# Optimization experiments

Measured on AMD Instinct MI355X. Metric: run time of the kernel, lower is better.

Reference implementation:

```python
import jax, jax.numpy as jnp
import numpy as np

B, S, D, H = 4, 1500, 1280, 20
HD = D // H  # 64

def setup_inputs() -> dict:
    key = jax.random.key(0)
    ks = jax.random.split(key, 8)
    scale = 1.0 / np.sqrt(D)
    return {
        "hidden_states": jax.random.normal(ks[0], (B, S, D), dtype=jnp.float32),
        "attention_mask": jnp.zeros((B, 1, S, S), dtype=jnp.float32),
        "q_w": jax.random.normal(ks[1], (D, D), dtype=jnp.float32) * scale,
        "q_b": jax.random.normal(ks[2], (D,), dtype=jnp.float32) * 0.02,
        "k_w": jax.random.normal(ks[3], (D, D), dtype=jnp.float32) * scale,
        "v_w": jax.random.normal(ks[4], (D, D), dtype=jnp.float32) * scale,
        "v_b": jax.random.normal(ks[5], (D,), dtype=jnp.float32) * 0.02,
        "o_w": jax.random.normal(ks[6], (D, D), dtype=jnp.float32) * scale,
        "o_b": jax.random.normal(ks[7], (D,), dtype=jnp.float32) * 0.02,
    }

def reference(hidden_states, attention_mask, q_w, q_b, k_w, v_w, v_b, o_w, o_b):
    bsz, seq_len, d_model = hidden_states.shape
    scaling = HD ** (-0.5)
    # Projections (k_proj has NO bias, matching the module)
    q = hidden_states @ q_w + q_b
    k = hidden_states @ k_w
    v = hidden_states @ v_w + v_b
    # [B, H, S, HD]
    q = q.reshape(bsz, seq_len, H, HD).transpose(0, 2, 1, 3)
    k = k.reshape(bsz, seq_len, H, HD).transpose(0, 2, 1, 3)
    v = v.reshape(bsz, seq_len, H, HD).transpose(0, 2, 1, 3)
    scores = jnp.einsum("bhqd,bhkd->bhqk", q, k) * scaling
    scores = scores + attention_mask
    attn = jax.nn.softmax(scores.astype(jnp.float32), axis=-1).astype(q.dtype)
    out = jnp.einsum("bhqk,bhkd->bhqd", attn, v)
    out = out.transpose(0, 2, 1, 3).reshape(bsz, seq_len, d_model)
    return out @ o_w + o_b
```

## Files before the change

### kernel.cpp

```cpp
#include <hip/hip_runtime.h>
#include <hip/hip_bf16.h>
#include <cstddef>

#define B_   4
#define S_   1500
#define D_   1280
#define H_   20
#define HD_  64
#define M_   (B_*S_)
#define SPAD 1536
#define BIGNEG (-1e30f)
#define LOG2E 1.44269504088896340736f
#define KVB  64
#define NTA  24

typedef short bf16x8 __attribute__((ext_vector_type(8)));
typedef float f32x4 __attribute__((ext_vector_type(4)));
typedef unsigned short u16;
typedef u16 u16x8 __attribute__((ext_vector_type(8)));
typedef unsigned int u32x4v __attribute__((ext_vector_type(4)));

#define MFMA __builtin_amdgcn_mfma_f32_16x16x32_bf16

__device__ __forceinline__ u16 f2bf(float f) {
  union { float f; unsigned u; } x; x.f = f;
  unsigned r = (x.u + 0x7fffu + ((x.u >> 16) & 1u)) >> 16;
  return (u16)r;
}

__device__ __forceinline__ unsigned cvtpk(float a, float b) {
  unsigned r;
  asm volatile("v_cvt_pk_bf16_f32 %0, %1, %2" : "=v"(r) : "v"(a), "v"(b));
  return r;
}

__device__ __forceinline__ void gl_lds16(const u16* g, u16* l) {
  typedef __attribute__((address_space(1))) const unsigned GU;
  typedef __attribute__((address_space(3))) unsigned LU;
  __builtin_amdgcn_global_load_lds((GU*)g, (LU*)l, 16, 0, 0);
}

__global__ __launch_bounds__(256) void k_conv(const float* __restrict__ X, u16* __restrict__ Y) {
  size_t i = (size_t)blockIdx.x * 256 + threadIdx.x;
  const float4* p = (const float4*)(X + i * 8);
  float4 a = p[0], b = p[1];
  u16x8 v;
  v[0]=f2bf(a.x); v[1]=f2bf(a.y); v[2]=f2bf(a.z); v[3]=f2bf(a.w);
  v[4]=f2bf(b.x); v[5]=f2bf(b.y); v[6]=f2bf(b.z); v[7]=f2bf(b.w);
  *(u16x8*)(Y + i * 8) = v;
}

__global__ __launch_bounds__(256) void k_trans4(const float* __restrict__ qw,
                                                const float* __restrict__ kw,
                                                const float* __restrict__ vw,
                                                const float* __restrict__ ow,
                                                u16* __restrict__ Wt) {
  const float* W = (blockIdx.z == 0) ? qw : (blockIdx.z == 1) ? kw
                   : (blockIdx.z == 2) ? vw : ow;
  u16* dst = Wt + (size_t)blockIdx.z * D_ * D_;
  __shared__ float t[32][33];
  int n0 = blockIdx.x * 32, k0 = blockIdx.y * 32;
  int tx = threadIdx.x & 31, ty = threadIdx.x >> 5;
  #pragma unroll
  for (int i = ty; i < 32; i += 8) t[i][tx] = W[(size_t)(k0 + i) * D_ + n0 + tx];
  __syncthreads();
  #pragma unroll
  for (int i = ty; i < 32; i += 8) dst[(size_t)(n0 + i) * D_ + k0 + tx] = f2bf(t[tx][i]);
}

__global__ __launch_bounds__(256) void k_vtrans(const u16* __restrict__ Vb, u16* __restrict__ Vt) {
  __shared__ u16 t[128][72];
  int bh = blockIdx.x, b = bh / H_, h = bh % H_;
  int s0 = blockIdx.y * 128;
  int tid = threadIdx.x;
  #pragma unroll
  for (int r = 0; r < 4; r++) {
    int sl = r * 32 + (tid >> 3);
    int s = s0 + sl; if (s > S_ - 1) s = S_ - 1;
    bf16x8 v = *(const bf16x8*)(Vb + ((size_t)(b * S_ + s)) * D_ + h * HD_ + (tid & 7) * 8);
    *(bf16x8*)&t[sl][(tid & 7) * 8] = v;
  }
  __syncthreads();
  #pragma unroll
  for (int r = 0; r < 4; r++) {
    int d = r * 16 + (tid >> 4);
    int ss = (tid & 15) * 8;
    u16x8 o;
    #pragma unroll
    for (int q = 0; q < 8; q++) {
      int sl = ss + q;
      int kk = ((sl >> 4) & 3) * 4 + (sl & 3) + ((sl >> 2) & 3) * 16 + (sl & 64);
      o[q] = t[kk][d];
    }
    *(u16x8*)(Vt + ((size_t)bh * HD_ + d) * SPAD + s0 + ss) = o;
  }
}

__global__ __launch_bounds__(256) void k_gemmqkv(const u16* __restrict__ A,
                                                 const u16* __restrict__ Wt,
                                                 const float* __restrict__ q_b,
                                                 const float* __restrict__ v_b,
                                                 u16* __restrict__ Qb) {
  __shared__ u16 As[2][128 * 64];
  __shared__ u16 Bs[2][128 * 64];
  int tid = threadIdx.x;
  int lane = tid & 63;
  int wv = tid >> 6;
  int l16 = lane & 15, lg = lane >> 4;
  int wr = wv >> 1, wc = wv & 1;
  int m0 = blockIdx.x * 128;
  int n0g = blockIdx.y * 128;
  int sel = blockIdx.y / 10;
  int nloc = n0g - sel * 1280;

  int srow = tid >> 3;
  int csw = ((tid & 7) ^ (srow & 7)) * 8;
  const u16* asrc = A + csw;
  const u16* bsrc = Wt + csw;
  int dbase = wv * 8 * 64;

  f32x4 acc[4][4] = {};

#define STAGEG(tt, bufb) do {                                            \
    int kk0 = (tt) * 64;                                                 \
    _Pragma("unroll")                                                    \
    for (int c = 0; c < 4; c++) {                                        \
      int row = srow + c * 32;                                           \
      int ar = m0 + row; if (ar > M_ - 1) ar = M_ - 1;                   \
      gl_lds16(asrc + (size_t)ar * D_ + kk0,                             \
               &As[bufb][0] + dbase + c * 2048);                         \
      gl_lds16(bsrc + (size_t)(n0g + row) * D_ + kk0,                    \
               &Bs[bufb][0] + dbase + c * 2048);                         \
    }                                                                    \
  } while (0)

  STAGEG(0, 0);
  __syncthreads();
  for (int t = 0; t < 20; t++) {
    int cb = t & 1;
    if (t < 19) STAGEG(t + 1, cb ^ 1);
    const u16* AsC = &As[cb][0];
    const u16* BsC = &Bs[cb][0];
    #pragma unroll
    for (int kk = 0; kk < 2; kk++) {
      int pcol = ((kk * 4 + lg) ^ (l16 & 7)) * 8;
      bf16x8 af[4], bf[4];
      #pragma unroll
      for (int m = 0; m < 4; m++)
        af[m] = *(const bf16x8*)&AsC[(wr * 64 + m * 16 + l16) * 64 + pcol];
      #pragma unroll
      for (int n = 0; n < 4; n++)
        bf[n] = *(const bf16x8*)&BsC[(wc * 64 + n * 16 + l16) * 64 + pcol];
      __builtin_amdgcn_s_setprio(1);
      #pragma unroll
      for (int m = 0; m < 4; m++)
        #pragma unroll
        for (int n = 0; n < 4; n++)
          acc[m][n] = MFMA(af[m], bf[n], acc[m][n], 0, 0, 0);
      __builtin_amdgcn_s_setprio(0);
    }
    __syncthreads();
  }
#undef STAGEG

  const float* bias = (sel == 0) ? q_b : v_b;
  float scl = (sel == 0) ? (0.125f * LOG2E) : 1.0f;
  u16* outb = Qb + (size_t)sel * ((size_t)M_ * D_);

  #pragma unroll
  for (int m = 0; m < 4; m++) {
    int row0 = m0 + wr * 64 + m * 16 + lg * 4;
    #pragma unroll
    for (int n = 0; n < 4; n++) {
      int colL = nloc + wc * 64 + n * 16 + l16;
      float bv = (sel == 1) ? 0.0f : bias[colL];
      #pragma unroll
      for (int j = 0; j < 4; j++) {
        int row = row0 + j;
        if (row < M_) {
          float v = (acc[m][n][j] + bv) * scl;
          outb[(size_t)row * D_ + colL] = f2bf(v);
        }
      }
    }
  }
}

__global__ __launch_bounds__(256) void k_gemmo(const u16* __restrict__ A,
                                               const u16* __restrict__ Wt,
                                               const float* __restrict__ bias,
                                               float* __restrict__ outp) {
  __shared__ u16 As[2][128 * 64];
  __shared__ u16 Bs[2][128 * 64];
  int tid = threadIdx.x;
  int lane = tid & 63;
  int wv = tid >> 6;
  int l16 = lane & 15, lg = lane >> 4;
  int wr = wv >> 1, wc = wv & 1;
  int m0 = blockIdx.x * 128, n0 = blockIdx.y * 128;

  int srow = tid >> 3;
  int csw = ((tid & 7) ^ (srow & 7)) * 8;
  const u16* asrc = A + csw;
  const u16* bsrc = Wt + csw;
  int dbase = wv * 8 * 64;

  f32x4 acc[4][4] = {};

#define STAGEG(tt, bufb) do {                                            \
    int kk0 = (tt) * 64;                                                 \
    _Pragma("unroll")                                                    \
    for (int c = 0; c < 4; c++) {                                        \
      int row = srow + c * 32;                                           \
      int ar = m0 + row; if (ar > M_ - 1) ar = M_ - 1;                   \
      gl_lds16(asrc + (size_t)ar * D_ + kk0,                             \
               &As[bufb][0] + dbase + c * 2048);                         \
      gl_lds16(bsrc + (size_t)(n0 + row) * D_ + kk0,                     \
               &Bs[bufb][0] + dbase + c * 2048);                         \
    }                                                                    \
  } while (0)

  STAGEG(0, 0);
  __syncthreads();
  for (int t = 0; t < 20; t++) {
    int cb = t & 1;
    if (t < 19) STAGEG(t + 1, cb ^ 1);
    const u16* AsC = &As[cb][0];
    const u16* BsC = &Bs[cb][0];
    #pragma unroll
    for (int kk = 0; kk < 2; kk++) {
      int pcol = ((kk * 4 + lg) ^ (l16 & 7)) * 8;
      bf16x8 af[4], bf[4];
      #pragma unroll
      for (int m = 0; m < 4; m++)
        af[m] = *(const bf16x8*)&AsC[(wr * 64 + m * 16 + l16) * 64 + pcol];
      #pragma unroll
      for (int n = 0; n < 4; n++)
        bf[n] = *(const bf16x8*)&BsC[(wc * 64 + n * 16 + l16) * 64 + pcol];
      __builtin_amdgcn_s_setprio(1);
      #pragma unroll
      for (int m = 0; m < 4; m++)
        #pragma unroll
        for (int n = 0; n < 4; n++)
          acc[m][n] = MFMA(af[m], bf[n], acc[m][n], 0, 0, 0);
      __builtin_amdgcn_s_setprio(0);
    }
    __syncthreads();
  }
#undef STAGEG

  #pragma unroll
  for (int m = 0; m < 4; m++) {
    int row0 = m0 + wr * 64 + m * 16 + lg * 4;
    #pragma unroll
    for (int n = 0; n < 4; n++) {
      int col = n0 + wc * 64 + n * 16 + l16;
      float bv = bias[col];
      #pragma unroll
      for (int j = 0; j < 4; j++) {
        int row = row0 + j;
        if (row < M_) outp[(size_t)row * D_ + col] = acc[m][n][j] + bv;
      }
    }
  }
}

__global__ __launch_bounds__(256) void k_attn(const u16* __restrict__ Qb,
                                              const u16* __restrict__ Kb,
                                              const u16* __restrict__ Vt,
                                              const float* __restrict__ mask,
                                              u16* __restrict__ Ctx) {
  __shared__ u16 Kl[2][64 * 64];
  __shared__ u16 Vl[2][64 * 64];

  int p = blockIdx.x;
  int L = (p & 7) * 240 + (p >> 3);
  int h = L % 20;
  int g = L / 20;
  int b = g / 24;
  int xq = g % 24;
  int bh = b * H_ + h;

  int tid = threadIdx.x;
  int lane = tid & 63, wv = tid >> 6;
  int l16 = lane & 15, lg = lane >> 4;
  int qw0 = xq * 64 + wv * 16;

  int qr = qw0 + l16; if (qr > S_ - 1) qr = S_ - 1;
  const u16* qp = Qb + ((size_t)(b * S_ + qr)) * D_ + h * HD_ + lg * 8;
  bf16x8 aq0 = *(const bf16x8*)(qp);
  bf16x8 aq1 = *(const bf16x8*)(qp + 32);
  const float* mrow = mask + (size_t)b * S_ * S_ + (size_t)qr * S_;

  int sr0 = wv * 16 + (lane >> 3);
  int csw = ((lane & 7) ^ (lane >> 3)) * 8;
  const u16* ksrc = Kb + (size_t)b * S_ * D_ + h * HD_ + csw;
  const u16* vsrc0 = Vt + ((size_t)bh * HD_ + sr0) * SPAD + csw;
  const u16* vsrc1 = vsrc0 + 8 * SPAD;

  float m_ = BIGNEG, l_ = 0.0f;
  f32x4 acc[4] = {};
  const f32x4 zf = {0, 0, 0, 0};
  float4 mvs[4];

#define STAGE(k0s, bufb) do {                                          \
    int key0_ = (k0s) + sr0;     if (key0_ > S_ - 1) key0_ = S_ - 1;   \
    int key1_ = key0_ + 8;       if (key1_ > S_ - 1) key1_ = S_ - 1;   \
    u16* kd_ = &Kl[bufb][0] + wv * 1024;                               \
    u16* vd_ = &Vl[bufb][0] + wv * 1024;                               \
    gl_lds16(ksrc + (size_t)key0_ * D_, kd_);                          \
    gl_lds16(ksrc + (size_t)key1_ * D_, kd_ + 512);                    \
    gl_lds16(vsrc0 + (k0s), vd_);                                      \
    gl_lds16(vsrc1 + (k0s), vd_ + 512);                                \
  } while (0)

#define COMPUTE(curb, k0_, LASTV) do {                                 \
    const u16* KlC = &Kl[curb][0];                                     \
    const u16* VlC = &Vl[curb][0];                                     \
    f32x4 s[4];                                                        \
    __builtin_amdgcn_s_setprio(1);                                     \
    _Pragma("unroll")                                                  \
    for (int sub = 0; sub < 4; sub++) {                                \
      const u16* kb = KlC + (sub * 16 + l16) * 64;                     \
      bf16x8 kf0 = *(const bf16x8*)(kb + ((lg     ^ (l16 & 7)) * 8));  \
      bf16x8 kf1 = *(const bf16x8*)(kb + (((4+lg) ^ (l16 & 7)) * 8));  \
      s[sub] = MFMA(kf0, aq0, zf, 0, 0, 0);                            \
      s[sub] = MFMA(kf1, aq1, s[sub], 0, 0, 0);                        \
    }                                                                  \
    __builtin_amdgcn_s_setprio(0);                                     \
    _Pragma("unroll")                                                  \
    for (int sub = 0; sub < 4; sub++) {                                \
      s[sub][0] = fmaf(mvs[sub].x, LOG2E, s[sub][0]);                  \
      s[sub][1] = fmaf(mvs[sub].y, LOG2E, s[sub][1]);                  \
      s[sub][2] = fmaf(mvs[sub].z, LOG2E, s[sub][2]);                  \
      s[sub][3] = fmaf(mvs[sub].w, LOG2E, s[sub][3]);                  \
    }                                                                  \
    if (LASTV) {                                                       \
      _Pragma("unroll")                                                \
      for (int sub = 0; sub < 4; sub++) {                              \
        int kb_ = (k0_) + sub * 16 + lg * 4;                           \
        _Pragma("unroll")                                              \
        for (int j = 0; j < 4; j++)                                    \
          if (kb_ + j >= S_) s[sub][j] = BIGNEG;                       \
      }                                                                \
    }                                                                  \
    float t0 = fmaxf(fmaxf(s[0][0], s[0][1]), fmaxf(s[0][2], s[0][3]));\
    float t1 = fmaxf(fmaxf(s[1][0], s[1][1]), fmaxf(s[1][2], s[1][3]));\
    float t2 = fmaxf(fmaxf(s[2][0], s[2][1]), fmaxf(s[2][2], s[2][3]));\
    float t3 = fmaxf(fmaxf(s[3][0], s[3][1]), fmaxf(s[3][2], s[3][3]));\
    float rmax = fmaxf(fmaxf(t0, t1), fmaxf(t2, t3));                  \
    rmax = fmaxf(rmax, __shfl_xor(rmax, 16));                          \
    rmax = fmaxf(rmax, __shfl_xor(rmax, 32));                          \
    float mn = fmaxf(m_, rmax);                                        \
    if (!__all(mn - m_ <= 8.0f)) {                                     \
      float c = __builtin_amdgcn_exp2f(m_ - mn);                       \
      m_ = mn; l_ *= c;                                                \
      _Pragma("unroll")                                                \
      for (int j = 0; j < 4; j++) {                                    \
        float cj = __shfl(c, lg * 4 + j);                              \
        acc[0][j] *= cj; acc[1][j] *= cj;                              \
        acc[2][j] *= cj; acc[3][j] *= cj;                              \
      }                                                                \
    }                                                                  \
    _Pragma("unroll")                                                  \
    for (int sub = 0; sub < 4; sub++)                                  \
      _Pragma("unroll")                                                \
      for (int j = 0; j < 4; j++)                                      \
        s[sub][j] = __builtin_amdgcn_exp2f(s[sub][j] - m_);            \
    float a0 = (s[0][0] + s[0][1]) + (s[0][2] + s[0][3]);              \
    float a1 = (s[1][0] + s[1][1]) + (s[1][2] + s[1][3]);              \
    float a2 = (s[2][0] + s[2][1]) + (s[2][2] + s[2][3]);              \
    float a3 = (s[3][0] + s[3][1]) + (s[3][2] + s[3][3]);              \
    float rs = (a0 + a1) + (a2 + a3);                                  \
    rs += __shfl_xor(rs, 16);                                          \
    rs += __shfl_xor(rs, 32);                                          \
    l_ += rs;                                                          \
    {                                                                  \
      union { u32x4v u; bf16x8 bf; } pc;                               \
      pc.u[0] = cvtpk(s[0][0], s[0][1]); pc.u[1] = cvtpk(s[0][2], s[0][3]); \
      pc.u[2] = cvtpk(s[1][0], s[1][1]); pc.u[3] = cvtpk(s[1][2], s[1][3]); \
      __builtin_amdgcn_s_setprio(1);                                   \
      _Pragma("unroll")                                                \
      for (int n = 0; n < 4; n++) {                                    \
        const u16* vb = VlC + (n * 16 + l16) * 64;                     \
        bf16x8 bv = *(const bf16x8*)(vb + (((lg*2  ) ^ (l16 & 7)) * 8)); \
        acc[n] = MFMA(pc.bf, bv, acc[n], 0, 0, 0);                     \
      }                                                                \
      __builtin_amdgcn_s_setprio(0);                                   \
    }                                                                  \
    {                                                                  \
      union { u32x4v u; bf16x8 bf; } pc;                               \
      pc.u[0] = cvtpk(s[2][0], s[2][1]); pc.u[1] = cvtpk(s[2][2], s[2][3]); \
      pc.u[2] = cvtpk(s[3][0], s[3][1]); pc.u[3] = cvtpk(s[3][2], s[3][3]); \
      __builtin_amdgcn_s_setprio(1);                                   \
      _Pragma("unroll")                                                \
      for (int n = 0; n < 4; n++) {                                    \
        const u16* vb = VlC + (n * 16 + l16) * 64;                     \
        bf16x8 bv = *(const bf16x8*)(vb + (((lg*2+1) ^ (l16 & 7)) * 8)); \
        acc[n] = MFMA(pc.bf, bv, acc[n], 0, 0, 0);                     \
      }                                                                \
      __builtin_amdgcn_s_setprio(0);                                   \
    }                                                                  \
  } while (0)

  STAGE(0, 0);

  for (int t = 0; t < NTA - 1; t++) {
    int k0 = t * KVB;
    #pragma unroll
    for (int sub = 0; sub < 4; sub++)
      mvs[sub] = *(const float4*)(mrow + k0 + sub * 16 + lg * 4);
    __builtin_amdgcn_s_barrier();
    asm volatile("" ::: "memory");
    STAGE(k0 + KVB, (t + 1) & 1);
    asm volatile("s_waitcnt vmcnt(4)" ::: "memory");
    __builtin_amdgcn_s_barrier();
    asm volatile("" ::: "memory");
    COMPUTE(t & 1, k0, false);
  }
  {
    const int k0 = (NTA - 1) * KVB;
    #pragma unroll
    for (int sub = 0; sub < 4; sub++) {
      int mc = k0 + sub * 16 + lg * 4; if (mc > S_ - 4) mc = S_ - 4;
      mvs[sub] = *(const float4*)(mrow + mc);
    }
    __builtin_amdgcn_s_barrier();
    asm volatile("s_waitcnt vmcnt(0)" ::: "memory");
    __builtin_amdgcn_s_barrier();
    asm volatile("" ::: "memory");
    COMPUTE((NTA - 1) & 1, k0, true);
  }

  float inv = 1.0f / l_;
  #pragma unroll
  for (int j = 0; j < 4; j++) {
    float invj = __shfl(inv, lg * 4 + j);
    int row = qw0 + lg * 4 + j;
    if (row < S_) {
      #pragma unroll
      for (int n = 0; n < 4; n++) {
        float v = acc[n][j] * invj;
        Ctx[((size_t)(b * S_ + row)) * D_ + h * HD_ + n * 16 + l16] = f2bf(v);
      }
    }
  }
#undef STAGE
#undef COMPUTE
}

extern "C" void kernel_launch(void* const* d_in, const int* in_sizes, int n_in,
                              void* d_out, int out_size, void* d_ws, size_t ws_size,
                              hipStream_t stream) {
  const float* hs   = (const float*)d_in[0];
  const float* mask = (const float*)d_in[1];
  const float* q_w  = (const float*)d_in[2];
  const float* q_b  = (const float*)d_in[3];
  const float* k_w  = (const float*)d_in[4];
  const float* v_w  = (const float*)d_in[5];
  const float* v_b  = (const float*)d_in[6];
  const float* o_w  = (const float*)d_in[7];
  const float* o_b  = (const float*)d_in[8];
  float* out = (float*)d_out;

  char* w = (char*)d_ws;
  const size_t XD = (size_t)M_ * D_;
  const size_t WD = (size_t)D_ * D_;
  u16* Xb  = (u16*)(w);                 w += XD * 2;
  u16* Wtq = (u16*)(w);                 w += WD * 2;
  u16* Wtk = (u16*)(w);                 w += WD * 2;
  u16* Wtv = (u16*)(w);                 w += WD * 2;
  u16* Wto = (u16*)(w);                 w += WD * 2;
  u16* Qb  = (u16*)(w);                 w += XD * 2;
  u16* Kb  = (u16*)(w);                 w += XD * 2;
  u16* Vb  = (u16*)(w);                 w += XD * 2;
  u16* Vt  = (u16*)(w);                 w += (size_t)B_ * H_ * HD_ * SPAD * 2;
  u16* Ctx = Xb;
  (void)Wtk; (void)Wtv;

  k_conv<<<dim3(3750), dim3(256), 0, stream>>>(hs, Xb);
  k_trans4<<<dim3(40, 40, 4), dim3(256), 0, stream>>>(q_w, k_w, v_w, o_w, Wtq);

  k_gemmqkv<<<dim3(47, 30), dim3(256), 0, stream>>>(Xb, Wtq, q_b, v_b, Qb);
  k_vtrans<<<dim3(80, 12), dim3(256), 0, stream>>>(Vb, Vt);

  k_attn<<<dim3(1920), dim3(256), 0, stream>>>(Qb, Kb, Vt, mask, Ctx);

  k_gemmo<<<dim3(47, 10), dim3(256), 0, stream>>>(Ctx, Wto, o_b, out);
}
```

Baseline: 276.9 us.

## Process two query tiles per attention block to reuse staged K/V

```diff
diff --git a/kernel.cpp b/kernel.cpp
--- a/kernel.cpp
+++ b/kernel.cpp
@@ -274,23 +274,28 @@
   __shared__ u16 Vl[2][64 * 64];
 
   int p = blockIdx.x;
-  int L = (p & 7) * 240 + (p >> 3);
+  int L = (p & 7) * 120 + (p >> 3);
   int h = L % 20;
   int g = L / 20;
-  int b = g / 24;
-  int xq = g % 24;
+  int b = g / 12;
+  int xq = g % 12;
   int bh = b * H_ + h;
 
   int tid = threadIdx.x;
   int lane = tid & 63, wv = tid >> 6;
   int l16 = lane & 15, lg = lane >> 4;
-  int qw0 = xq * 64 + wv * 16;
-
-  int qr = qw0 + l16; if (qr > S_ - 1) qr = S_ - 1;
-  const u16* qp = Qb + ((size_t)(b * S_ + qr)) * D_ + h * HD_ + lg * 8;
-  bf16x8 aq0 = *(const bf16x8*)(qp);
-  bf16x8 aq1 = *(const bf16x8*)(qp + 32);
-  const float* mrow = mask + (size_t)b * S_ * S_ + (size_t)qr * S_;
+  int qw0 = xq * 128 + wv * 16;
+
+  int qr0 = qw0 + l16;      if (qr0 > S_ - 1) qr0 = S_ - 1;
+  int qr1 = qw0 + 64 + l16; if (qr1 > S_ - 1) qr1 = S_ - 1;
+  const u16* qp0 = Qb + ((size_t)(b * S_ + qr0)) * D_ + h * HD_ + lg * 8;
+  const u16* qp1 = Qb + ((size_t)(b * S_ + qr1)) * D_ + h * HD_ + lg * 8;
+  bf16x8 aq00 = *(const bf16x8*)(qp0);
+  bf16x8 aq01 = *(const bf16x8*)(qp0 + 32);
+  bf16x8 aq10 = *(const bf16x8*)(qp1);
+  bf16x8 aq11 = *(const bf16x8*)(qp1 + 32);
+  const float* mrow0 = mask + (size_t)b * S_ * S_ + (size_t)qr0 * S_;
+  const float* mrow1 = mask + (size_t)b * S_ * S_ + (size_t)qr1 * S_;
 
   int sr0 = wv * 16 + (lane >> 3);
   int csw = ((lane & 7) ^ (lane >> 3)) * 8;
@@ -298,8 +303,8 @@
   const u16* vsrc0 = Vt + ((size_t)bh * HD_ + sr0) * SPAD + csw;
   const u16* vsrc1 = vsrc0 + 8 * SPAD;
 
-  float m_ = BIGNEG, l_ = 0.0f;
-  f32x4 acc[4] = {};
+  float m0_ = BIGNEG, l0_ = 0.0f, m1_ = BIGNEG, l1_ = 0.0f;
+  f32x4 acc0[4] = {}, acc1[4] = {};
   const f32x4 zf = {0, 0, 0, 0};
   float4 mvs[4];
 
@@ -314,26 +319,70 @@
     gl_lds16(vsrc1 + (k0s), vd_ + 512);                                \
   } while (0)
 
+#define SMX(sv, mm, ll, accv) do {                                     \
+    float t0 = fmaxf(fmaxf(sv[0][0], sv[0][1]), fmaxf(sv[0][2], sv[0][3])); \
+    float t1 = fmaxf(fmaxf(sv[1][0], sv[1][1]), fmaxf(sv[1][2], sv[1][3])); \
+    float t2 = fmaxf(fmaxf(sv[2][0], sv[2][1]), fmaxf(sv[2][2], sv[2][3])); \
+    float t3 = fmaxf(fmaxf(sv[3][0], sv[3][1]), fmaxf(sv[3][2], sv[3][3])); \
+    float rmax = fmaxf(fmaxf(t0, t1), fmaxf(t2, t3));                  \
+    rmax = fmaxf(rmax, __shfl_xor(rmax, 16));                          \
+    rmax = fmaxf(rmax, __shfl_xor(rmax, 32));                          \
+    float mn = fmaxf(mm, rmax);                                        \
+    if (!__all(mn - mm <= 8.0f)) {                                     \
+      float c = __builtin_amdgcn_exp2f(mm - mn);                       \
+      mm = mn; ll *= c;                                                \
+      _Pragma("unroll")                                                \
+      for (int j = 0; j < 4; j++) {                                    \
+        float cj = __shfl(c, lg * 4 + j);                              \
+        accv[0][j] *= cj; accv[1][j] *= cj;                            \
+        accv[2][j] *= cj; accv[3][j] *= cj;                            \
+      }                                                                \
+    }                                                                  \
+    _Pragma("unroll")                                                  \
+    for (int sub = 0; sub < 4; sub++)                                  \
+      _Pragma("unroll")                                                \
+      for (int j = 0; j < 4; j++)                                      \
+        sv[sub][j] = __builtin_amdgcn_exp2f(sv[sub][j] - mm);          \
+    float a0 = (sv[0][0] + sv[0][1]) + (sv[0][2] + sv[0][3]);          \
+    float a1 = (sv[1][0] + sv[1][1]) + (sv[1][2] + sv[1][3]);          \
+    float a2 = (sv[2][0] + sv[2][1]) + (sv[2][2] + sv[2][3]);          \
+    float a3 = (sv[3][0] + sv[3][1]) + (sv[3][2] + sv[3][3]);          \
+    float rs = (a0 + a1) + (a2 + a3);                                  \
+    rs += __shfl_xor(rs, 16);                                          \
+    rs += __shfl_xor(rs, 32);                                          \
+    ll += rs;                                                          \
+  } while (0)
+
 #define COMPUTE(curb, k0_, LASTV) do {                                 \
     const u16* KlC = &Kl[curb][0];                                     \
     const u16* VlC = &Vl[curb][0];                                     \
-    f32x4 s[4];                                                        \
+    f32x4 s0[4], s1[4];                                                \
     __builtin_amdgcn_s_setprio(1);                                     \
     _Pragma("unroll")                                                  \
     for (int sub = 0; sub < 4; sub++) {                                \
       const u16* kb = KlC + (sub * 16 + l16) * 64;                     \
       bf16x8 kf0 = *(const bf16x8*)(kb + ((lg     ^ (l16 & 7)) * 8));  \
       bf16x8 kf1 = *(const bf16x8*)(kb + (((4+lg) ^ (l16 & 7)) * 8));  \
-      s[sub] = MFMA(kf0, aq0, zf, 0, 0, 0);                            \
-      s[sub] = MFMA(kf1, aq1, s[sub], 0, 0, 0);                        \
+      s0[sub] = MFMA(kf0, aq00, zf, 0, 0, 0);                          \
+      s0[sub] = MFMA(kf1, aq01, s0[sub], 0, 0, 0);                     \
+      s1[sub] = MFMA(kf0, aq10, zf, 0, 0, 0);                          \
+      s1[sub] = MFMA(kf1, aq11, s1[sub], 0, 0, 0);                     \
     }                                                                  \
     __builtin_amdgcn_s_setprio(0);                                     \
+     \
+    float4 mv1[4];                                                     \
     _Pragma("unroll")                                                  \
     for (int sub = 0; sub < 4; sub++) {                                \
-      s[sub][0] = fmaf(mvs[sub].x, LOG2E, s[sub][0]);                  \
-      s[sub][1] = fmaf(mvs[sub].y, LOG2E, s[sub][1]);                  \
-      s[sub][2] = fmaf(mvs[sub].z, LOG2E, s[sub][2]);                  \
-      s[sub][3] = fmaf(mvs[sub].w, LOG2E, s[sub][3]);                  \
+      int mc = (k0_) + sub * 16 + lg * 4;                              \
+      if (LASTV && mc > S_ - 4) mc = S_ - 4;                           \
+      mv1[sub] = *(const float4*)(mrow1 + mc);                         \
+    }                                                                  \
+    _Pragma("unroll")                                                  \
+    for (int sub = 0; sub < 4; sub++) {                                \
+      s0[sub][0] = fmaf(mvs[sub].x, LOG2E, s0[sub][0]);                \
+      s0[sub][1] = fmaf(mvs[sub].y, LOG2E, s0[sub][1]);                \
+      s0[sub][2] = fmaf(mvs[sub].z, LOG2E, s0[sub][2]);                \
+      s0[sub][3] = fmaf(mvs[sub].w, LOG2E, s0[sub][3]);                \
     }                                                                  \
     if (LASTV) {                                                       \
       _Pragma("unroll")                                                \
@@ -341,66 +390,49 @@
         int kb_ = (k0_) + sub * 16 + lg * 4;                           \
         _Pragma("unroll")                                              \
         for (int j = 0; j < 4; j++)                                    \
-          if (kb_ + j >= S_) s[sub][j] = BIGNEG;                       \
+          if (kb_ + j >= S_) s0[sub][j] = BIGNEG;                      \
       }                                                                \
     }                                                                  \
-    float t0 = fmaxf(fmaxf(s[0][0], s[0][1]), fmaxf(s[0][2], s[0][3]));\
-    float t1 = fmaxf(fmaxf(s[1][0], s[1][1]), fmaxf(s[1][2], s[1][3]));\
-    float t2 = fmaxf(fmaxf(s[2][0], s[2][1]), fmaxf(s[2][2], s[2][3]));\
-    float t3 = fmaxf(fmaxf(s[3][0], s[3][1]), fmaxf(s[3][2], s[3][3]));\
-    float rmax = fmaxf(fmaxf(t0, t1), fmaxf(t2, t3));                  \
-    rmax = fmaxf(rmax, __shfl_xor(rmax, 16));                          \
-    rmax = fmaxf(rmax, __shfl_xor(rmax, 32));                          \
-    float mn = fmaxf(m_, rmax);                                        \
-    if (!__all(mn - m_ <= 8.0f)) {                                     \
-      float c = __builtin_amdgcn_exp2f(m_ - mn);                       \
-      m_ = mn; l_ *= c;                                                \
+    SMX(s0, m0_, l0_, acc0);                                           \
+    union { u32x4v u; bf16x8 bf; } pA0, pA1;                           \
+    pA0.u[0] = cvtpk(s0[0][0], s0[0][1]); pA0.u[1] = cvtpk(s0[0][2], s0[0][3]); \
+    pA0.u[2] = cvtpk(s0[1][0], s0[1][1]); pA0.u[3] = cvtpk(s0[1][2], s0[1][3]); \
+    pA1.u[0] = cvtpk(s0[2][0], s0[2][1]); pA1.u[1] = cvtpk(s0[2][2], s0[2][3]); \
+    pA1.u[2] = cvtpk(s0[3][0], s0[3][1]); pA1.u[3] = cvtpk(s0[3][2], s0[3][3]); \
+    _Pragma("unroll")                                                  \
+    for (int sub = 0; sub < 4; sub++) {                                \
+      s1[sub][0] = fmaf(mv1[sub].x, LOG2E, s1[sub][0]);                \
+      s1[sub][1] = fmaf(mv1[sub].y, LOG2E, s1[sub][1]);                \
+      s1[sub][2] = fmaf(mv1[sub].z, LOG2E, s1[sub][2]);                \
+      s1[sub][3] = fmaf(mv1[sub].w, LOG2E, s1[sub][3]);                \
+    }                                                                  \
+    if (LASTV) {                                                       \
       _Pragma("unroll")                                                \
-      for (int j = 0; j < 4; j++) {                                    \
-        float cj = __shfl(c, lg * 4 + j);                              \
-        acc[0][j] *= cj; acc[1][j] *= cj;                              \
-        acc[2][j] *= cj; acc[3][j] *= cj;                              \
+      for (int sub = 0; sub < 4; sub++) {                              \
+        int kb_ = (k0_) + sub * 16 + lg * 4;                           \
+        _Pragma("unroll")                                              \
+        for (int j = 0; j < 4; j++)                                    \
+          if (kb_ + j >= S_) s1[sub][j] = BIGNEG;                      \
       }                                                                \
     }                                                                  \
+    SMX(s1, m1_, l1_, acc1);                                           \
+    union { u32x4v u; bf16x8 bf; } pB0, pB1;                           \
+    pB0.u[0] = cvtpk(s1[0][0], s1[0][1]); pB0.u[1] = cvtpk(s1[0][2], s1[0][3]); \
+    pB0.u[2] = cvtpk(s1[1][0], s1[1][1]); pB0.u[3] = cvtpk(s1[1][2], s1[1][3]); \
+    pB1.u[0] = cvtpk(s1[2][0], s1[2][1]); pB1.u[1] = cvtpk(s1[2][2], s1[2][3]); \
+    pB1.u[2] = cvtpk(s1[3][0], s1[3][1]); pB1.u[3] = cvtpk(s1[3][2], s1[3][3]); \
+    __builtin_amdgcn_s_setprio(1);                                     \
     _Pragma("unroll")                                                  \
-    for (int sub = 0; sub < 4; sub++)                                  \
-      _Pragma("unroll")                                                \
-      for (int j = 0; j < 4; j++)                                      \
-        s[sub][j] = __builtin_amdgcn_exp2f(s[sub][j] - m_);            \
-    float a0 = (s[0][0] + s[0][1]) + (s[0][2] + s[0][3]);              \
-    float a1 = (s[1][0] + s[1][1]) + (s[1][2] + s[1][3]);              \
-    float a2 = (s[2][0] + s[2][1]) + (s[2][2] + s[2][3]);              \
-    float a3 = (s[3][0] + s[3][1]) + (s[3][2] + s[3][3]);              \
-    float rs = (a0 + a1) + (a2 + a3);                                  \
-    rs += __shfl_xor(rs, 16);                                          \
-    rs += __shfl_xor(rs, 32);                                          \
-    l_ += rs;                                                          \
-    {                                                                  \
-      union { u32x4v u; bf16x8 bf; } pc;                               \
-      pc.u[0] = cvtpk(s[0][0], s[0][1]); pc.u[1] = cvtpk(s[0][2], s[0][3]); \
-      pc.u[2] = cvtpk(s[1][0], s[1][1]); pc.u[3] = cvtpk(s[1][2], s[1][3]); \
-      __builtin_amdgcn_s_setprio(1);                                   \
-      _Pragma("unroll")                                                \
-      for (int n = 0; n < 4; n++) {                                    \
-        const u16* vb = VlC + (n * 16 + l16) * 64;                     \
-        bf16x8 bv = *(const bf16x8*)(vb + (((lg*2  ) ^ (l16 & 7)) * 8)); \
-        acc[n] = MFMA(pc.bf, bv, acc[n], 0, 0, 0);                     \
-      }                                                                \
-      __builtin_amdgcn_s_setprio(0);                                   \
-    }                                                                  \
-    {                                                                  \
-      union { u32x4v u; bf16x8 bf; } pc;                               \
-      pc.u[0] = cvtpk(s[2][0], s[2][1]); pc.u[1] = cvtpk(s[2][2], s[2][3]); \
-      pc.u[2] = cvtpk(s[3][0], s[3][1]); pc.u[3] = cvtpk(s[3][2], s[3][3]); \
-      __builtin_amdgcn_s_setprio(1);                                   \
-      _Pragma("unroll")                                                \
-      for (int n = 0; n < 4; n++) {                                    \
-        const u16* vb = VlC + (n * 16 + l16) * 64;                     \
-        bf16x8 bv = *(const bf16x8*)(vb + (((lg*2+1) ^ (l16 & 7)) * 8)); \
-        acc[n] = MFMA(pc.bf, bv, acc[n], 0, 0, 0);                     \
-      }                                                                \
-      __builtin_amdgcn_s_setprio(0);                                   \
-    }                                                                  \
+    for (int n = 0; n < 4; n++) {                                      \
+      const u16* vb = VlC + (n * 16 + l16) * 64;                       \
+      bf16x8 bv0 = *(const bf16x8*)(vb + (((lg*2  ) ^ (l16 & 7)) * 8));\
+      bf16x8 bv1 = *(const bf16x8*)(vb + (((lg*2+1) ^ (l16 & 7)) * 8));\
+      acc0[n] = MFMA(pA0.bf, bv0, acc0[n], 0, 0, 0);                   \
+      acc0[n] = MFMA(pA1.bf, bv1, acc0[n], 0, 0, 0);                   \
+      acc1[n] = MFMA(pB0.bf, bv0, acc1[n], 0, 0, 0);                   \
+      acc1[n] = MFMA(pB1.bf, bv1, acc1[n], 0, 0, 0);                   \
+    }                                                                  \
+    __builtin_amdgcn_s_setprio(0);                                     \
   } while (0)
 
   STAGE(0, 0);
@@ -409,7 +441,7 @@
     int k0 = t * KVB;
     #pragma unroll
     for (int sub = 0; sub < 4; sub++)
-      mvs[sub] = *(const float4*)(mrow + k0 + sub * 16 + lg * 4);
+      mvs[sub] = *(const float4*)(mrow0 + k0 + sub * 16 + lg * 4);
     __builtin_amdgcn_s_barrier();
     asm volatile("" ::: "memory");
     STAGE(k0 + KVB, (t + 1) & 1);
@@ -423,7 +455,7 @@
     #pragma unroll
     for (int sub = 0; sub < 4; sub++) {
       int mc = k0 + sub * 16 + lg * 4; if (mc > S_ - 4) mc = S_ - 4;
-      mvs[sub] = *(const float4*)(mrow + mc);
+      mvs[sub] = *(const float4*)(mrow0 + mc);
     }
     __builtin_amdgcn_s_barrier();
     asm volatile("s_waitcnt vmcnt(0)" ::: "memory");
@@ -432,20 +464,27 @@
     COMPUTE((NTA - 1) & 1, k0, true);
   }
 
-  float inv = 1.0f / l_;
+  float inv0 = 1.0f / l0_;
+  float inv1 = 1.0f / l1_;
   #pragma unroll
   for (int j = 0; j < 4; j++) {
-    float invj = __shfl(inv, lg * 4 + j);
-    int row = qw0 + lg * 4 + j;
-    if (row < S_) {
-      #pragma unroll
-      for (int n = 0; n < 4; n++) {
-        float v = acc[n][j] * invj;
-        Ctx[((size_t)(b * S_ + row)) * D_ + h * HD_ + n * 16 + l16] = f2bf(v);
-      }
+    float ivj0 = __shfl(inv0, lg * 4 + j);
+    float ivj1 = __shfl(inv1, lg * 4 + j);
+    int row0 = qw0 + lg * 4 + j;
+    int row1 = row0 + 64;
+    if (row0 < S_) {
+      #pragma unroll
+      for (int n = 0; n < 4; n++)
+        Ctx[((size_t)(b * S_ + row0)) * D_ + h * HD_ + n * 16 + l16] = f2bf(acc0[n][j] * ivj0);
+    }
+    if (row1 < S_) {
+      #pragma unroll
+      for (int n = 0; n < 4; n++)
+        Ctx[((size_t)(b * S_ + row1)) * D_ + h * HD_ + n * 16 + l16] = f2bf(acc1[n][j] * ivj1);
     }
   }
 #undef STAGE
+#undef SMX
 #undef COMPUTE
 }
 
@@ -484,7 +523,7 @@
   k_gemmqkv<<<dim3(47, 30), dim3(256), 0, stream>>>(Xb, Wtq, q_b, v_b, Qb);
   k_vtrans<<<dim3(80, 12), dim3(256), 0, stream>>>(Vb, Vt);
 
-  k_attn<<<dim3(1920), dim3(256), 0, stream>>>(Qb, Kb, Vt, mask, Ctx);
+  k_attn<<<dim3(960), dim3(256), 0, stream>>>(Qb, Kb, Vt, mask, Ctx);
 
   k_gemmo<<<dim3(47, 10), dim3(256), 0, stream>>>(Ctx, Wto, o_b, out);
 }
```

Measured after the change: 271.9 us. Within noise of the previous version (-1.8%).
